# Kernel optimization log

Measured on AMD Instinct MI355X. Metric: run time of the kernel, lower is better.

## Reference

```python
import jax, jax.numpy as jnp
import numpy as np

EPS = 1e-8

def _cdist(a, b):
    # Euclidean pairwise distances, torch.cdist(p=2) equivalent.
    sq = (jnp.sum(a * a, axis=1)[:, None] + jnp.sum(b * b, axis=1)[None, :]
          - 2.0 * (a @ b.T))
    return jnp.sqrt(jnp.maximum(sq, 1e-12))

def setup_inputs() -> dict:
    key = jax.random.key(0)
    k1, k2, k3, k4, k5, k6 = jax.random.split(key, 6)
    ns, n_cls, n_feat, K = 4096, 500, 256, 400
    return {
        "src_x": jax.random.normal(k1, (ns, n_feat), dtype=jnp.float32),
        "tgt_x": jax.random.normal(k2, (ns, n_feat), dtype=jnp.float32),
        "src_y": jax.random.uniform(k3, (ns, n_cls), dtype=jnp.float32),
        "tgt_y": jax.random.uniform(k4, (ns, n_cls), dtype=jnp.float32),
        "queue": jax.random.normal(k5, (n_cls, n_feat, K), dtype=jnp.float32),
        "queue_size": jax.random.randint(k6, (n_cls,), 0, K, dtype=jnp.int32),
    }

def reference(src_x, tgt_x, src_y, tgt_y, queue, queue_size):
    n_cls, n_feat, K = queue.shape
    num = queue_size.astype(queue.dtype)[:, None]                      # (C,1)
    # src_centroid: masked mean over the first queue_size[c] columns
    valid = (jnp.arange(K)[None, :] < queue_size[:, None]).astype(queue.dtype)  # (C,K)
    centroid = jnp.einsum('cfk,ck->cf', queue, valid) / jnp.maximum(num, 1.0)
    centroid = jnp.where(num > 0, centroid, 0.0)                       # (C,F)

    batch_src = src_y.T @ src_x                                        # (C,F)
    total_num = num + jnp.sum(src_y, axis=0)[:, None] + EPS            # (C,1)
    mean_src = (centroid * num + batch_src) / total_num                # (C,F)

    batch_prob = jnp.sum(tgt_y, axis=0)[:, None] + EPS                 # (C,1)
    mean_tgt = (tgt_y.T @ tgt_x) / batch_prob                          # (C,F)

    intra = jnp.diagonal(_cdist(mean_src, mean_tgt)).mean()
    inter = _cdist(mean_src, mean_src).mean()
    return intra, inter
```

## Files before the change

### kernel.cpp

```cpp
#include <hip/hip_runtime.h>
#include <math.h>

#define NS 4096
#define NC 500
#define NF 256
#define NK 400
#define KC_GEMM 16
#define KC_CS   32

#define NB_GEMM (32 * KC_GEMM * 2)
#define NB_CS   (KC_CS * 2)
#define NB_OTH  (NB_GEMM + NB_CS)
#define NB_QUE  ((NC * NF) / 32)

__global__ __launch_bounds__(256) void k_heavy(
    const float* __restrict__ Xs, const float* __restrict__ Ys, float* __restrict__ Ps,
    const float* __restrict__ Xt, const float* __restrict__ Yt, float* __restrict__ Pt,
    float* __restrict__ CSs, float* __restrict__ CSt,
    const float* __restrict__ queue, const int* __restrict__ qsize,
    float* __restrict__ qsum) {
  __shared__ float ytile[NS / KC_GEMM][16];
  const int bid = blockIdx.x;

  if (bid < NB_GEMM) {
    const int z   = bid >> 9;
    const int rem = bid & 511;
    const int kc  = rem >> 5;
    const int c0  = (rem & 31) * 16;
    const float* X = z ? Xt : Xs;
    const float* Y = z ? Yt : Ys;
    float*       P = z ? Pt : Ps;
    const int n0   = kc * (NS / KC_GEMM);
    const int cmax = (NC - c0 < 16) ? (NC - c0) : 16;

    for (int i = threadIdx.x; i < (NS / KC_GEMM) * 16; i += 256) {
      int rr = i >> 4, cc = i & 15;
      ytile[rr][cc] = (cc < cmax) ? Y[(size_t)(n0 + rr) * NC + c0 + cc] : 0.f;
    }
    __syncthreads();

    const int f = threadIdx.x;
    float acc[16];
    #pragma unroll
    for (int j = 0; j < 16; ++j) acc[j] = 0.f;

    #pragma unroll 4
    for (int n = 0; n < NS / KC_GEMM; ++n) {
      float xv = X[(size_t)(n0 + n) * NF + f];
      #pragma unroll
      for (int j = 0; j < 16; ++j) acc[j] = fmaf(ytile[n][j], xv, acc[j]);
    }
    #pragma unroll
    for (int j = 0; j < 16; ++j)
      if (c0 + j < NC) P[((size_t)kc * NC + c0 + j) * NF + f] = acc[j];

  } else if (bid < NB_OTH) {
    const int b = bid - NB_GEMM;
    const float* Y = (b >> 5) ? Yt : Ys;
    float*      CS = (b >> 5) ? CSt : CSs;
    const int kc = b & 31;
    const int n0 = kc * (NS / KC_CS);
    const int t  = threadIdx.x;
    float s0 = 0.f, s1 = 0.f;
    for (int n = n0; n < n0 + NS / KC_CS; ++n) {
      const float* row = Y + (size_t)n * NC;
      s0 += row[t];
      if (t + 256 < NC) s1 += row[t + 256];
    }
    CS[kc * 512 + t] = s0;
    if (t + 256 < NC) CS[kc * 512 + t + 256] = s1;

  } else {
    const int qb   = bid - NB_OTH;
    const int widx = threadIdx.x >> 6;
    const int lane = threadIdx.x & 63;
    const int r0   = (qb * 4 + widx) * 8;
    const int c    = r0 >> 8;
    const int qs   = qsize[c];
    const int L    = (qs + 3) >> 2;
    const float* base = queue + (size_t)r0 * NK;
    float s0 = 0.f, s1 = 0.f, s2 = 0.f, s3 = 0.f;
    float s4 = 0.f, s5 = 0.f, s6 = 0.f, s7 = 0.f;

    if (lane < L) {
      const int k = 4 * lane;
      float4 v0 = *reinterpret_cast<const float4*>(base + 0 * NK + k);
      float4 v1 = *reinterpret_cast<const float4*>(base + 1 * NK + k);
      float4 v2 = *reinterpret_cast<const float4*>(base + 2 * NK + k);
      float4 v3 = *reinterpret_cast<const float4*>(base + 3 * NK + k);
      float4 v4 = *reinterpret_cast<const float4*>(base + 4 * NK + k);
      float4 v5 = *reinterpret_cast<const float4*>(base + 5 * NK + k);
      float4 v6 = *reinterpret_cast<const float4*>(base + 6 * NK + k);
      float4 v7 = *reinterpret_cast<const float4*>(base + 7 * NK + k);
      s0 += v0.x; s1 += v1.x; s2 += v2.x; s3 += v3.x;
      s4 += v4.x; s5 += v5.x; s6 += v6.x; s7 += v7.x;
      if (k + 1 < qs) { s0 += v0.y; s1 += v1.y; s2 += v2.y; s3 += v3.y;
                        s4 += v4.y; s5 += v5.y; s6 += v6.y; s7 += v7.y; }
      if (k + 2 < qs) { s0 += v0.z; s1 += v1.z; s2 += v2.z; s3 += v3.z;
                        s4 += v4.z; s5 += v5.z; s6 += v6.z; s7 += v7.z; }
      if (k + 3 < qs) { s0 += v0.w; s1 += v1.w; s2 += v2.w; s3 += v3.w;
                        s4 += v4.w; s5 += v5.w; s6 += v6.w; s7 += v7.w; }
    }
    if (lane + 64 < L) {
      const int k = 256 + 4 * lane;
      float4 v0 = *reinterpret_cast<const float4*>(base + 0 * NK + k);
      float4 v1 = *reinterpret_cast<const float4*>(base + 1 * NK + k);
      float4 v2 = *reinterpret_cast<const float4*>(base + 2 * NK + k);
      float4 v3 = *reinterpret_cast<const float4*>(base + 3 * NK + k);
      float4 v4 = *reinterpret_cast<const float4*>(base + 4 * NK + k);
      float4 v5 = *reinterpret_cast<const float4*>(base + 5 * NK + k);
      float4 v6 = *reinterpret_cast<const float4*>(base + 6 * NK + k);
      float4 v7 = *reinterpret_cast<const float4*>(base + 7 * NK + k);
      s0 += v0.x; s1 += v1.x; s2 += v2.x; s3 += v3.x;
      s4 += v4.x; s5 += v5.x; s6 += v6.x; s7 += v7.x;
      if (k + 1 < qs) { s0 += v0.y; s1 += v1.y; s2 += v2.y; s3 += v3.y;
                        s4 += v4.y; s5 += v5.y; s6 += v6.y; s7 += v7.y; }
      if (k + 2 < qs) { s0 += v0.z; s1 += v1.z; s2 += v2.z; s3 += v3.z;
                        s4 += v4.z; s5 += v5.z; s6 += v6.z; s7 += v7.z; }
      if (k + 3 < qs) { s0 += v0.w; s1 += v1.w; s2 += v2.w; s3 += v3.w;
                        s4 += v4.w; s5 += v5.w; s6 += v6.w; s7 += v7.w; }
    }
    #pragma unroll
    for (int m = 32; m; m >>= 1) {
      s0 += __shfl_xor(s0, m); s1 += __shfl_xor(s1, m);
      s2 += __shfl_xor(s2, m); s3 += __shfl_xor(s3, m);
      s4 += __shfl_xor(s4, m); s5 += __shfl_xor(s5, m);
      s6 += __shfl_xor(s6, m); s7 += __shfl_xor(s7, m);
    }
    if (lane == 0) {
      *reinterpret_cast<float4*>(&qsum[r0])     = make_float4(s0, s1, s2, s3);
      *reinterpret_cast<float4*>(&qsum[r0 + 4]) = make_float4(s4, s5, s6, s7);
    }
  }
}

__global__ __launch_bounds__(256) void k_means(
    const float* __restrict__ qsum, const int* __restrict__ qsize,
    const float* __restrict__ Psrc, const float* __restrict__ Ptgt,
    const float* __restrict__ CSsrc, const float* __restrict__ CStgt,
    float* __restrict__ MS, float* __restrict__ MT, float* __restrict__ ipart) {
  const int c = blockIdx.x * 4 + (threadIdx.x >> 6);
  const int lane = threadIdx.x & 63;
  const int f4 = lane * 4;
  if (c >= NC) return;

  float cs_s = 0.f, cs_t = 0.f;
  #pragma unroll
  for (int kc = 0; kc < KC_CS; ++kc) {
    cs_s += CSsrc[kc * 512 + c];
    cs_t += CStgt[kc * 512 + c];
  }
  float num = (float)qsize[c];
  float4 ns = *reinterpret_cast<const float4*>(&qsum[(size_t)c * NF + f4]);
  float4 nt = make_float4(0.f, 0.f, 0.f, 0.f);
  #pragma unroll
  for (int kc = 0; kc < KC_GEMM; ++kc) {
    float4 ps = *reinterpret_cast<const float4*>(&Psrc[((size_t)kc * NC + c) * NF + f4]);
    float4 pt = *reinterpret_cast<const float4*>(&Ptgt[((size_t)kc * NC + c) * NF + f4]);
    ns.x += ps.x; ns.y += ps.y; ns.z += ps.z; ns.w += ps.w;
    nt.x += pt.x; nt.y += pt.y; nt.z += pt.z; nt.w += pt.w;
  }
  float rs = 1.f / (num + cs_s + 1e-8f);
  float rt = 1.f / (cs_t + 1e-8f);
  float4 ms = make_float4(ns.x * rs, ns.y * rs, ns.z * rs, ns.w * rs);
  float4 mt = make_float4(nt.x * rt, nt.y * rt, nt.z * rt, nt.w * rt);
  *reinterpret_cast<float4*>(&MS[(size_t)c * NF + f4]) = ms;
  *reinterpret_cast<float4*>(&MT[(size_t)c * NF + f4]) = mt;

  float dx = ms.x - mt.x, dy = ms.y - mt.y, dz = ms.z - mt.z, dw = ms.w - mt.w;
  float s = dx * dx + dy * dy + dz * dz + dw * dw;
  #pragma unroll
  for (int m = 32; m; m >>= 1) s += __shfl_xor(s, m);
  if (lane == 0) ipart[c] = sqrtf(fmaxf(s, 1e-12f));
}

#define TC 16
#define NBT 32
__global__ __launch_bounds__(256) void k_dist(const float* __restrict__ MS,
                                              float* __restrict__ epart) {
  __shared__ float a[TC][NF + 4];
  __shared__ float b[TC][NF + 4];
  const int bi = blockIdx.x & (NBT - 1);
  const int bj = blockIdx.x >> 5;

  for (int i = threadIdx.x; i < TC * (NF / 4); i += 256) {
    int rr = i >> 6, fq = (i & 63) * 4;
    int c1 = bi * TC + rr;
    int c2 = bj * TC + rr;
    float4 va = (c1 < NC) ? *reinterpret_cast<const float4*>(&MS[(size_t)c1 * NF + fq])
                          : make_float4(0.f, 0.f, 0.f, 0.f);
    float4 vb = (c2 < NC) ? *reinterpret_cast<const float4*>(&MS[(size_t)c2 * NF + fq])
                          : make_float4(0.f, 0.f, 0.f, 0.f);
    *reinterpret_cast<float4*>(&a[rr][fq]) = va;
    *reinterpret_cast<float4*>(&b[rr][fq]) = vb;
  }
  __syncthreads();

  const int i1 = threadIdx.x >> 4, i2 = threadIdx.x & 15;
  float s = 0.f;
  #pragma unroll 8
  for (int fq = 0; fq < NF; fq += 4) {
    float4 va = *reinterpret_cast<const float4*>(&a[i1][fq]);
    float4 vb = *reinterpret_cast<const float4*>(&b[i2][fq]);
    float d0 = va.x - vb.x, d1 = va.y - vb.y, d2 = va.z - vb.z, d3 = va.w - vb.w;
    s = fmaf(d0, d0, s); s = fmaf(d1, d1, s); s = fmaf(d2, d2, s); s = fmaf(d3, d3, s);
  }
  bool valid = (bi * TC + i1 < NC) && (bj * TC + i2 < NC);
  float rr = valid ? sqrtf(fmaxf(s, 1e-12f)) : 0.f;

  #pragma unroll
  for (int m = 32; m; m >>= 1) rr += __shfl_xor(rr, m);
  __shared__ float red[4];
  int wid = threadIdx.x >> 6, lane = threadIdx.x & 63;
  if (lane == 0) red[wid] = rr;
  __syncthreads();
  if (threadIdx.x == 0) epart[blockIdx.x] = red[0] + red[1] + red[2] + red[3];
}

__global__ __launch_bounds__(1024) void k_final(const float* __restrict__ ipart,
                                                const float* __restrict__ epart,
                                                float* __restrict__ out) {
  const int t = threadIdx.x;
  float si = (t < NC) ? ipart[t] : 0.f;
  float se = epart[t];
  #pragma unroll
  for (int m = 32; m; m >>= 1) { si += __shfl_xor(si, m); se += __shfl_xor(se, m); }
  __shared__ float ri[16], re[16];
  int wid = t >> 6, lane = t & 63;
  if (lane == 0) { ri[wid] = si; re[wid] = se; }
  __syncthreads();
  if (t == 0) {
    float A = 0.f, B = 0.f;
    #pragma unroll
    for (int w = 0; w < 16; ++w) { A += ri[w]; B += re[w]; }
    out[0] = A / (float)NC;
    out[1] = B / ((float)NC * (float)NC);
  }
}

extern "C" void kernel_launch(void* const* d_in, const int* in_sizes, int n_in,
                              void* d_out, int out_size, void* d_ws, size_t ws_size,
                              hipStream_t stream) {
  const float* src_x = (const float*)d_in[0];
  const float* tgt_x = (const float*)d_in[1];
  const float* src_y = (const float*)d_in[2];
  const float* tgt_y = (const float*)d_in[3];
  const float* queue = (const float*)d_in[4];
  const int*   qsize = (const int*)d_in[5];
  float* out = (float*)d_out;

  float* ws    = (float*)d_ws;
  float* qsum  = ws;
  float* Psrc  = qsum + NC * NF;
  float* Ptgt  = Psrc + (size_t)KC_GEMM * NC * NF;
  float* CSs   = Ptgt + (size_t)KC_GEMM * NC * NF;
  float* CSt   = CSs + KC_CS * 512;
  float* MS    = CSt + KC_CS * 512;
  float* MT    = MS + NC * NF;
  float* ipart = MT + NC * NF;
  float* epart = ipart + NC;

  k_heavy<<<NB_OTH + NB_QUE, 256, 0, stream>>>(
      src_x, src_y, Psrc, tgt_x, tgt_y, Ptgt, CSs, CSt, queue, qsize, qsum);

  k_means<<<(NC + 3) / 4, 256, 0, stream>>>(qsum, qsize, Psrc, Ptgt, CSs, CSt, MS, MT, ipart);

  k_dist<<<NBT * NBT, 256, 0, stream>>>(MS, epart);

  k_final<<<1, 1024, 0, stream>>>(ipart, epart, out);
}
```

Baseline: 75.83 us.

## Retile GEMM partial sums as 4x4 register blocks and widen k_means grid

The class-by-feature partial GEMM now gives each wave 4 classes and each lane 4 consecutive features. It uses float4 loads of X and a broadcast float4 read of the Y tile, replacing the old scheme where each thread held one feature and looped over 16 classes. This cuts LDS reads per FMA and vectorizes the global loads and stores, but each block now reads the X tile four times (once per wave), likely from cache. k_means switches to one 256-thread block per class with scalar loads and a shared-memory reduction, giving more blocks but narrower loads.

```diff
diff --git a/kernel.cpp b/kernel.cpp
--- a/kernel.cpp
+++ b/kernel.cpp
@@ -19,8 +19,11 @@
     float* __restrict__ CSs, float* __restrict__ CSt,
     const float* __restrict__ queue, const int* __restrict__ qsize,
     float* __restrict__ qsum) {
-  __shared__ float ytile[NS / KC_GEMM][16];
-  const int bid = blockIdx.x;
+  __shared__ float ytile[256][16];
+  const int bid  = blockIdx.x;
+  const int tid  = threadIdx.x;
+  const int w    = tid >> 6;
+  const int lane = tid & 63;
 
   if (bid < NB_GEMM) {
     const int z   = bid >> 9;
@@ -30,29 +33,42 @@
     const float* X = z ? Xt : Xs;
     const float* Y = z ? Yt : Ys;
     float*       P = z ? Pt : Ps;
-    const int n0   = kc * (NS / KC_GEMM);
+    const int n0   = kc * 256;
     const int cmax = (NC - c0 < 16) ? (NC - c0) : 16;
 
-    for (int i = threadIdx.x; i < (NS / KC_GEMM) * 16; i += 256) {
+    for (int i = tid; i < 256 * 16; i += 256) {
       int rr = i >> 4, cc = i & 15;
       ytile[rr][cc] = (cc < cmax) ? Y[(size_t)(n0 + rr) * NC + c0 + cc] : 0.f;
     }
     __syncthreads();
 
-    const int f = threadIdx.x;
-    float acc[16];
-    #pragma unroll
-    for (int j = 0; j < 16; ++j) acc[j] = 0.f;
+    const int cg = w;
+    const int f4 = lane * 4;
+    float4 a0 = make_float4(0.f, 0.f, 0.f, 0.f);
+    float4 a1 = make_float4(0.f, 0.f, 0.f, 0.f);
+    float4 a2 = make_float4(0.f, 0.f, 0.f, 0.f);
+    float4 a3 = make_float4(0.f, 0.f, 0.f, 0.f);
+    const float* Xp = X + (size_t)n0 * NF + f4;
 
     #pragma unroll 4
-    for (int n = 0; n < NS / KC_GEMM; ++n) {
-      float xv = X[(size_t)(n0 + n) * NF + f];
-      #pragma unroll
-      for (int j = 0; j < 16; ++j) acc[j] = fmaf(ytile[n][j], xv, acc[j]);
-    }
-    #pragma unroll
-    for (int j = 0; j < 16; ++j)
-      if (c0 + j < NC) P[((size_t)kc * NC + c0 + j) * NF + f] = acc[j];
+    for (int n = 0; n < 256; ++n) {
+      float4 xv = *reinterpret_cast<const float4*>(Xp + (size_t)n * NF);
+      float4 yv = *reinterpret_cast<const float4*>(&ytile[n][cg * 4]);
+      a0.x = fmaf(yv.x, xv.x, a0.x); a0.y = fmaf(yv.x, xv.y, a0.y);
+      a0.z = fmaf(yv.x, xv.z, a0.z); a0.w = fmaf(yv.x, xv.w, a0.w);
+      a1.x = fmaf(yv.y, xv.x, a1.x); a1.y = fmaf(yv.y, xv.y, a1.y);
+      a1.z = fmaf(yv.y, xv.z, a1.z); a1.w = fmaf(yv.y, xv.w, a1.w);
+      a2.x = fmaf(yv.z, xv.x, a2.x); a2.y = fmaf(yv.z, xv.y, a2.y);
+      a2.z = fmaf(yv.z, xv.z, a2.z); a2.w = fmaf(yv.z, xv.w, a2.w);
+      a3.x = fmaf(yv.w, xv.x, a3.x); a3.y = fmaf(yv.w, xv.y, a3.y);
+      a3.z = fmaf(yv.w, xv.z, a3.z); a3.w = fmaf(yv.w, xv.w, a3.w);
+    }
+
+    float* Pb = &P[((size_t)kc * NC + c0 + cg * 4) * NF + f4];
+    if (c0 + cg * 4 + 0 < NC) *reinterpret_cast<float4*>(Pb + 0 * NF) = a0;
+    if (c0 + cg * 4 + 1 < NC) *reinterpret_cast<float4*>(Pb + 1 * NF) = a1;
+    if (c0 + cg * 4 + 2 < NC) *reinterpret_cast<float4*>(Pb + 2 * NF) = a2;
+    if (c0 + cg * 4 + 3 < NC) *reinterpret_cast<float4*>(Pb + 3 * NF) = a3;
 
   } else if (bid < NB_OTH) {
     const int b = bid - NB_GEMM;
@@ -60,7 +76,7 @@
     float*      CS = (b >> 5) ? CSt : CSs;
     const int kc = b & 31;
     const int n0 = kc * (NS / KC_CS);
-    const int t  = threadIdx.x;
+    const int t  = tid;
     float s0 = 0.f, s1 = 0.f;
     for (int n = n0; n < n0 + NS / KC_CS; ++n) {
       const float* row = Y + (size_t)n * NC;
@@ -71,13 +87,11 @@
     if (t + 256 < NC) CS[kc * 512 + t + 256] = s1;
 
   } else {
-    const int qb   = bid - NB_OTH;
-    const int widx = threadIdx.x >> 6;
-    const int lane = threadIdx.x & 63;
-    const int r0   = (qb * 4 + widx) * 8;
-    const int c    = r0 >> 8;
-    const int qs   = qsize[c];
-    const int L    = (qs + 3) >> 2;
+    const int qb = bid - NB_OTH;
+    const int r0 = (qb * 4 + w) * 8;
+    const int c  = r0 >> 8;
+    const int qs = qsize[c];
+    const int L  = (qs + 3) >> 2;
     const float* base = queue + (size_t)r0 * NK;
     float s0 = 0.f, s1 = 0.f, s2 = 0.f, s3 = 0.f;
     float s4 = 0.f, s5 = 0.f, s6 = 0.f, s7 = 0.f;
@@ -139,10 +153,8 @@
     const float* __restrict__ Psrc, const float* __restrict__ Ptgt,
     const float* __restrict__ CSsrc, const float* __restrict__ CStgt,
     float* __restrict__ MS, float* __restrict__ MT, float* __restrict__ ipart) {
-  const int c = blockIdx.x * 4 + (threadIdx.x >> 6);
-  const int lane = threadIdx.x & 63;
-  const int f4 = lane * 4;
-  if (c >= NC) return;
+  const int c = blockIdx.x;
+  const int f = threadIdx.x;
 
   float cs_s = 0.f, cs_t = 0.f;
   #pragma unroll
@@ -151,27 +163,27 @@
     cs_t += CStgt[kc * 512 + c];
   }
   float num = (float)qsize[c];
-  float4 ns = *reinterpret_cast<const float4*>(&qsum[(size_t)c * NF + f4]);
-  float4 nt = make_float4(0.f, 0.f, 0.f, 0.f);
+  float ns = qsum[(size_t)c * NF + f];
+  float nt = 0.f;
   #pragma unroll
   for (int kc = 0; kc < KC_GEMM; ++kc) {
-    float4 ps = *reinterpret_cast<const float4*>(&Psrc[((size_t)kc * NC + c) * NF + f4]);
-    float4 pt = *reinterpret_cast<const float4*>(&Ptgt[((size_t)kc * NC + c) * NF + f4]);
-    ns.x += ps.x; ns.y += ps.y; ns.z += ps.z; ns.w += ps.w;
-    nt.x += pt.x; nt.y += pt.y; nt.z += pt.z; nt.w += pt.w;
-  }
-  float rs = 1.f / (num + cs_s + 1e-8f);
-  float rt = 1.f / (cs_t + 1e-8f);
-  float4 ms = make_float4(ns.x * rs, ns.y * rs, ns.z * rs, ns.w * rs);
-  float4 mt = make_float4(nt.x * rt, nt.y * rt, nt.z * rt, nt.w * rt);
-  *reinterpret_cast<float4*>(&MS[(size_t)c * NF + f4]) = ms;
-  *reinterpret_cast<float4*>(&MT[(size_t)c * NF + f4]) = mt;
-
-  float dx = ms.x - mt.x, dy = ms.y - mt.y, dz = ms.z - mt.z, dw = ms.w - mt.w;
-  float s = dx * dx + dy * dy + dz * dz + dw * dw;
+    ns += Psrc[((size_t)kc * NC + c) * NF + f];
+    nt += Ptgt[((size_t)kc * NC + c) * NF + f];
+  }
+  float ms = ns / (num + cs_s + 1e-8f);
+  float mt = nt / (cs_t + 1e-8f);
+  MS[(size_t)c * NF + f] = ms;
+  MT[(size_t)c * NF + f] = mt;
+
+  float d = ms - mt;
+  float s = d * d;
   #pragma unroll
   for (int m = 32; m; m >>= 1) s += __shfl_xor(s, m);
-  if (lane == 0) ipart[c] = sqrtf(fmaxf(s, 1e-12f));
+  __shared__ float red[4];
+  int wid = f >> 6, lane = f & 63;
+  if (lane == 0) red[wid] = s;
+  __syncthreads();
+  if (f == 0) ipart[c] = sqrtf(fmaxf(red[0] + red[1] + red[2] + red[3], 1e-12f));
 }
 
 #define TC 16
@@ -232,7 +244,7 @@
   if (t == 0) {
     float A = 0.f, B = 0.f;
     #pragma unroll
-    for (int w = 0; w < 16; ++w) { A += ri[w]; B += re[w]; }
+    for (int w2 = 0; w2 < 16; ++w2) { A += ri[w2]; B += re[w2]; }
     out[0] = A / (float)NC;
     out[1] = B / ((float)NC * (float)NC);
   }
@@ -263,7 +275,7 @@
   k_heavy<<<NB_OTH + NB_QUE, 256, 0, stream>>>(
       src_x, src_y, Psrc, tgt_x, tgt_y, Ptgt, CSs, CSt, queue, qsize, qsum);
 
-  k_means<<<(NC + 3) / 4, 256, 0, stream>>>(qsum, qsize, Psrc, Ptgt, CSs, CSt, MS, MT, ipart);
+  k_means<<<NC, 256, 0, stream>>>(qsum, qsize, Psrc, Ptgt, CSs, CSt, MS, MT, ipart);
 
   k_dist<<<NBT * NBT, 256, 0, stream>>>(MS, epart);
 
```

Result: slower. 100.7 us (+32.7%).
